# Kernel tuning notes

Measured on AMD Instinct MI355X. Metric: run time of the kernel, lower is better.

The kernel has to match this reference:

```python
import jax, jax.numpy as jnp
import numpy as np

B, T, C = 8, 1024, 1024
H, HS = 16, 64            # n_head, head_size
K, STRIDE = 32, 16        # block_length, stride_length
WIN = 128                 # local_window_size
EPS = 1e-5


def _ln(z, w):
    m = jnp.mean(z, axis=-1, keepdims=True)
    v = jnp.var(z, axis=-1, keepdims=True)
    return (z - m) / jnp.sqrt(v + EPS) * w


def setup_inputs() -> dict:
    key = jax.random.key(0)
    ks = jax.random.split(key, 8)
    s = 0.02
    return {
        "x": jax.random.normal(ks[0], (B, T, C), jnp.float32),
        "c_attn_w": jax.random.normal(ks[1], (3 * C, C), jnp.float32) * s,
        "conv_w": jax.random.normal(ks[2], (HS, HS, K), jnp.float32) * s,
        "ln_comp_w": jnp.ones((HS,), jnp.float32),
        "ln_local_w": jnp.ones((C,), jnp.float32),
        "gate_w1": jax.random.normal(ks[3], (C, 2 * C), jnp.float32) * s,
        "gate_ln_w": jnp.ones((C,), jnp.float32),
        "gate_w2": jax.random.normal(ks[4], (2, C), jnp.float32) * s,
        "c_proj_w": jax.random.normal(ks[5], (C, C), jnp.float32) * s,
    }


def reference(x, c_attn_w, conv_w, ln_comp_w, ln_local_w, gate_w1, gate_ln_w, gate_w2, c_proj_w):
    qkv = jnp.einsum('btc,oc->bto', x, c_attn_w)          # [B,T,3C]
    q, k, v = jnp.split(qkv, 3, axis=-1)
    def heads(t):
        return t.reshape(B, T, H, HS).transpose(0, 2, 1, 3)  # [B,H,T,hs]
    q, k, v = heads(q), heads(k), heads(v)

    # CompressionMLP: Conv1d over time + LayerNorm(hs) + exact GELU
    def compress(t):
        xr = t.transpose(0, 1, 3, 2).reshape(B * H, HS, T)   # [B*H, hs, T]
        co = jax.lax.conv_general_dilated(
            xr, conv_w, window_strides=(STRIDE,), padding='VALID',
            dimension_numbers=('NCH', 'OIH', 'NCH'))          # [B*H, hs, NB]
        co = co.transpose(0, 2, 1)                            # [B*H, NB, hs]
        co = jax.nn.gelu(_ln(co, ln_comp_w), approximate=False)
        nb = co.shape[1]
        return co.reshape(B, H, nb, HS)

    kc = compress(k)
    vc = compress(v)
    NB = kc.shape[2]  # 63
    scale = 1.0 / np.sqrt(HS)

    ti = jnp.arange(T)
    band = (ti[None, :] <= ti[:, None]) & (ti[None, :] >= ti[:, None] - WIN)  # [T,T]
    s_loc = jnp.einsum('bhqd,bhkd->bhqk', q, k) * scale
    s_loc = jnp.where(band[None, None], s_loc, -jnp.inf)
    local_out = jnp.einsum('bhqk,bhkd->bhqd', jax.nn.softmax(s_loc, axis=-1), v)
    local_out = local_out.transpose(0, 2, 1, 3).reshape(B, T, C)
    local_norm = _ln(local_out, ln_local_w)

    # compressed-KV attention with block-causal mask: block j <= token i
    bj = jnp.arange(NB)
    cmask = bj[None, :] <= ti[:, None]                        # [T,NB]
    s_cmp = jnp.einsum('bhqd,bhkd->bhqk', q, kc) * scale
    s_cmp = jnp.where(cmask[None, None], s_cmp, -jnp.inf)
    comp_out = jnp.einsum('bhqk,bhkd->bhqd', jax.nn.softmax(s_cmp, axis=-1), vc)
    comp_out = comp_out.transpose(0, 2, 1, 3).reshape(B, T, C)

    # AttentionGating: last-token features -> Linear -> LN -> ReLU -> Linear -> softmax
    feats = jnp.concatenate([local_norm[:, -1, :], comp_out[:, -1, :]], axis=-1)  # [B,2C]
    h = jax.nn.relu(_ln(feats @ gate_w1.T, gate_ln_w))
    gates = jax.nn.softmax(h @ gate_w2.T, axis=-1)            # [B,2]

    combined = gates[:, None, 0:1] * local_norm + gates[:, None, 1:2] * comp_out
    y = jnp.einsum('btc,oc->bto', combined, c_proj_w)
    return y
```

## Files before the change

kernel.cpp:

```cpp
#include <hip/hip_runtime.h>
#include <cstdint>
#include <cmath>
#include <cstddef>

typedef unsigned int u32;
typedef unsigned short u16;
typedef __bf16 bf16x8 __attribute__((ext_vector_type(8)));
typedef float f32x4 __attribute__((ext_vector_type(4)));
typedef u32 u32x4 __attribute__((ext_vector_type(4)));
typedef u32 u32x2 __attribute__((ext_vector_type(2)));

#define DEV static __device__ __forceinline__

DEV float bflo(u32 u) { return __uint_as_float(u << 16); }
DEV float bfhi(u32 u) { return __uint_as_float(u & 0xffff0000u); }
DEV u16 f2bf(float f) {
  u32 u = __float_as_uint(f);
  u += 0x7fffu + ((u >> 16) & 1u);
  return (u16)(u >> 16);
}
DEV f32x4 unpack_bf4(u32x2 r) {
  return (f32x4){bflo(r[0]), bfhi(r[0]), bflo(r[1]), bfhi(r[1])};
}
DEV float wredsum(float v) {
#pragma unroll
  for (int o = 32; o; o >>= 1) v += __shfl_xor(v, o, 64);
  return v;
}

DEV void gload_lds16(const u16* g, u16* lds_base) {
  __builtin_amdgcn_global_load_lds((const __attribute__((address_space(1))) void*)g,
                                   (__attribute__((address_space(3))) void*)lds_base,
                                   16, 0, 0);
}

__global__ __launch_bounds__(256) void fused_cast(const float* __restrict__ x,
                                                  const float* __restrict__ aw,
                                                  const float* __restrict__ pw,
                                                  const float* __restrict__ cw,
                                                  u16* __restrict__ xb,
                                                  u16* __restrict__ wab,
                                                  u16* __restrict__ wpb,
                                                  u16* __restrict__ wcb,
                                                  u16* __restrict__ kcb,
                                                  u16* __restrict__ vcb) {
  const int blk = blockIdx.x;
  if (blk < 12288) {
    const float* src;
    u16* dst;
    int base;
    if (blk < 8192) { src = x; dst = xb; base = blk; }
    else if (blk < 11264) { src = aw; dst = wab; base = blk - 8192; }
    else { src = pw; dst = wpb; base = blk - 11264; }
    const size_t idx = ((size_t)base * 256 + threadIdx.x) * 4;
    const f32x4 v = *(const f32x4*)&src[idx];
    u32x2 r;
    r[0] = (u32)f2bf(v[0]) | ((u32)f2bf(v[1]) << 16);
    r[1] = (u32)f2bf(v[2]) | ((u32)f2bf(v[3]) << 16);
    *(u32x2*)&dst[idx] = r;
  } else if (blk < 12800) {
    const int idx = (blk - 12288) * 256 + threadIdx.x;
    const int o = idx >> 11;
    const int rest = idx & 2047;
    const int i = rest >> 5;
    const int kk = rest & 31;
    wcb[(o << 11) + (kk << 6) + i] = f2bf(cw[idx]);
  } else {
    for (int i = threadIdx.x; i < 8192; i += 256) {
      const int bh = i >> 6, d = i & 63;
      kcb[bh * 4096 + 63 * 64 + d] = 0;
      vcb[bh * 4096 + d * 64 + 63] = 0;
    }
  }
}

template <int OUT_BF16>
__global__ __launch_bounds__(256, 4) void gemm_bt(const u16* __restrict__ A,
                                                  const u16* __restrict__ Bm,
                                                  void* __restrict__ out,
                                                  int M, int N, int K) {
  __shared__ u16 As[128 * 64];
  __shared__ u16 Bs[128 * 64];
  const int tid = threadIdx.x;
  const int lane = tid & 63;
  const int w = tid >> 6;
  const int row0 = blockIdx.x * 128;
  const int col0 = blockIdx.y * 128;
  const int wm = (w >> 1) * 64, wn = (w & 1) * 64;
  const int lr = lane & 15, lq = lane >> 4;
  const int srow = lane >> 3;
  const int scol = ((lane & 7) ^ (srow & 7)) * 8;
  const int pgA = ((lq ^ (lr & 7)) * 8);

  f32x4 acc[4][4] = {};

  for (int k0 = 0; k0 < K; k0 += 64) {
    __syncthreads();
#pragma unroll
    for (int c = 0; c < 4; ++c) {
      const int base_r = w * 32 + c * 8;
      gload_lds16(&A[(size_t)(row0 + base_r + srow) * K + k0 + scol], &As[base_r * 64]);
      gload_lds16(&Bm[(size_t)(col0 + base_r + srow) * K + k0 + scol], &Bs[base_r * 64]);
    }
    __syncthreads();
#pragma unroll
    for (int ks = 0; ks < 2; ++ks) {
      const int pg = pgA ^ (ks << 5);
      bf16x8 af[4], bfr[4];
#pragma unroll
      for (int i = 0; i < 4; ++i) {
        af[i] = *(const bf16x8*)&As[(wm + i * 16 + lr) * 64 + pg];
        bfr[i] = *(const bf16x8*)&Bs[(wn + i * 16 + lr) * 64 + pg];
      }
#pragma unroll
      for (int i = 0; i < 4; ++i)
#pragma unroll
        for (int j = 0; j < 4; ++j)
          acc[i][j] = __builtin_amdgcn_mfma_f32_16x16x32_bf16(af[i], bfr[j], acc[i][j], 0, 0, 0);
    }
  }
#pragma unroll
  for (int i = 0; i < 4; ++i)
#pragma unroll
    for (int j = 0; j < 4; ++j)
#pragma unroll
      for (int rr = 0; rr < 4; ++rr) {
        const int gr = row0 + wm + i * 16 + lq * 4 + rr;
        const int gc = col0 + wn + j * 16 + lr;
        const float v = acc[i][j][rr];
        if (OUT_BF16)
          ((u16*)out)[(size_t)gr * N + gc] = f2bf(v);
        else
          ((float*)out)[(size_t)gr * N + gc] = v;
      }
}

__global__ __launch_bounds__(256) void compress_kernel(const u16* __restrict__ qkv,
                                                       const u16* __restrict__ Wc,
                                                       const float* __restrict__ ln_w,
                                                       u16* __restrict__ kcb,
                                                       u16* __restrict__ vcb) {
  __shared__ u16 As[2][32 * 128];
  __shared__ u16 Bs[2][64 * 128];
  __shared__ float Cs[32][65];
  const int tid = threadIdx.x;
  const int lane = tid & 63, w = tid >> 6;
  const int lr = lane & 15, lq = lane >> 4;
  const int r0 = blockIdx.x * 32;
  const int srcoff = 1024 + (int)blockIdx.y * 1024;

  size_t abase[2];
#pragma unroll
  for (int g2 = 0; g2 < 2; ++g2) {
    const int r = 8 * w + 4 * g2 + (lane >> 4);
    const int gr = r0 + r;
    const int bh = gr / 63;
    const int nb = gr - bh * 63;
    const int b = bh >> 4, h = bh & 15;
    const int jbit = (lane >> 3) & 1;
    const int icol = ((lane & 7) ^ (r & 7)) * 8;
    abase[g2] = (size_t)(b * 1024 + nb * 16 + jbit) * 3072 + srcoff + h * 64 + icol;
  }
  size_t bbase[4];
#pragma unroll
  for (int c = 0; c < 4; ++c) {
    const int rB = 16 * w + 4 * c + (lane >> 4);
    const int Lcol = (((lane & 7) ^ (rB & 7)) | (lane & 8)) * 8;
    bbase[c] = (size_t)rB * 2048 + Lcol;
  }

  auto stage = [&](int it, int bs) {
#pragma unroll
    for (int g2 = 0; g2 < 2; ++g2)
      gload_lds16(&qkv[abase[g2] + (size_t)it * 6144], &As[bs][(8 * w + 4 * g2) * 128]);
#pragma unroll
    for (int c = 0; c < 4; ++c)
      gload_lds16(&Wc[bbase[c] + (size_t)it * 128], &Bs[bs][(16 * w + 4 * c) * 128]);
  };

  const int rw = (w & 1) * 16;
  const int cw = (w >> 1) * 32;
  f32x4 acc[2] = {};

  stage(0, 0);
  for (int it = 0; it < 16; ++it) {
    const int cur = it & 1;
    __syncthreads();
    if (it < 15) stage(it + 1, cur ^ 1);
    const int rowA = rw + lr;
#pragma unroll
    for (int ks = 0; ks < 4; ++ks) {
      const int L = ks * 4 + lq;
      const int pgA = (((L & 7) ^ (rowA & 7)) | (L & 8)) * 8;
      const bf16x8 af = *(const bf16x8*)&As[cur][rowA * 128 + pgA];
#pragma unroll
      for (int j = 0; j < 2; ++j) {
        const int rowB = cw + j * 16 + lr;
        const int pgB = (((L & 7) ^ (rowB & 7)) | (L & 8)) * 8;
        const bf16x8 bfr = *(const bf16x8*)&Bs[cur][rowB * 128 + pgB];
        acc[j] = __builtin_amdgcn_mfma_f32_16x16x32_bf16(af, bfr, acc[j], 0, 0, 0);
      }
    }
  }
  __syncthreads();
#pragma unroll
  for (int j = 0; j < 2; ++j)
#pragma unroll
    for (int rr = 0; rr < 4; ++rr)
      Cs[rw + lq * 4 + rr][cw + j * 16 + lr] = acc[j][rr];
  __syncthreads();
  if (tid < 32) {
    const int gr2 = r0 + tid;
    const int bh2 = gr2 / 63;
    const int nb2 = gr2 - bh2 * 63;
    float s = 0.f, s2 = 0.f;
#pragma unroll 8
    for (int d = 0; d < 64; ++d) {
      const float xv = Cs[tid][d];
      s += xv;
      s2 += xv * xv;
    }
    const float m = s * (1.f / 64.f);
    const float inv = rsqrtf(s2 * (1.f / 64.f) - m * m + 1e-5f);
    if (blockIdx.y == 0) {
      const size_t gb = (size_t)bh2 * 4096 + nb2 * 64;
#pragma unroll 8
      for (int d = 0; d < 64; ++d) {
        const float z = (Cs[tid][d] - m) * inv * ln_w[d];
        kcb[gb + d] = f2bf(0.5f * z * (1.f + erff(z * 0.70710678118f)));
      }
    } else {
      const size_t gb = (size_t)bh2 * 4096 + nb2;
#pragma unroll 8
      for (int d = 0; d < 64; ++d) {
        const float z = (Cs[tid][d] - m) * inv * ln_w[d];
        vcb[gb + d * 64] = f2bf(0.5f * z * (1.f + erff(z * 0.70710678118f)));
      }
    }
  }
}

__global__ __launch_bounds__(256, 4) void attn_fused(const u16* __restrict__ qkv,
                                                     const u16* __restrict__ kcb,
                                                     const u16* __restrict__ vcb,
                                                     u16* __restrict__ loc,
                                                     u16* __restrict__ outc) {
  __shared__ __align__(16) char smem[40448];
  u16* Ks = (u16*)smem;
  u16* Ps = (u16*)smem;
  u16* Vt = (u16*)(smem + 27648);
  u16* Kc = (u16*)smem;
  u16* Vc = (u16*)(smem + 9216);
  u16* Pc = (u16*)(smem + 18432);
  const int bh = blockIdx.x;
  const int b = bh >> 4, h = bh & 15;
  const int i0 = blockIdx.y * 64;
  const int jbase = i0 - 128;
  const int tid = threadIdx.x;
  const int lane = tid & 63, w = tid >> 6;
  const int lr = lane & 15, lq = lane >> 4;
  const int j3 = lane & 3;
  const int dh1 = (lane >> 2) & 1;

  u32x4 vreg[6];
#pragma unroll
  for (int c = 0; c < 6; ++c) {
    const int lin = c * 256 + tid;
    const int s = lin >> 3, d0 = (lin & 7) * 8;
    const int j = jbase + s;
    u32x4 kval = {0, 0, 0, 0}, vval = {0, 0, 0, 0};
    if (j >= 0) {
      const size_t ro = (size_t)(b * 1024 + j) * 3072 + h * 64 + d0;
      kval = *(const u32x4*)&qkv[ro + 1024];
      vval = *(const u32x4*)&qkv[ro + 2048];
    }
    vreg[c] = vval;
    *(u32x4*)&Ks[s * 72 + d0] = kval;
  }
  if (!dh1) {
    const int d0 = (lane & 7) * 8;
#pragma unroll
    for (int c = 0; c < 6; ++c) {
      const int s = (c * 256 + tid) >> 3;
      const int sc = (((s >> 3) ^ j3) << 3) + (s & 7);
      const u32x4 val = vreg[c];
#pragma unroll
      for (int q = 0; q < 4; ++q) {
        Vt[(d0 + 2 * q) * 200 + sc] = (u16)(val[q] & 0xffffu);
        Vt[(d0 + 2 * q + 1) * 200 + sc] = (u16)(val[q] >> 16);
      }
    }
  }
  bf16x8 qf[2];
  {
    const size_t qrow = (size_t)(b * 1024 + i0 + w * 16 + lr) * 3072 + h * 64;
#pragma unroll
    for (int ks = 0; ks < 2; ++ks) qf[ks] = *(const bf16x8*)&qkv[qrow + ks * 32 + lq * 8];
  }
  const size_t cb = (size_t)bh * 4096;
  u32x4 kcreg[2], vcreg[2];
#pragma unroll
  for (int c2 = 0; c2 < 2; ++c2) {
    const int i2 = c2 * 256 + tid;
    const size_t o2 = (size_t)(i2 >> 3) * 64 + (i2 & 7) * 8;
    kcreg[c2] = *(const u32x4*)&kcb[cb + o2];
    vcreg[c2] = *(const u32x4*)&vcb[cb + o2];
  }
  __syncthreads();

  f32x4 sa[9];
#pragma unroll
  for (int j9 = 0; j9 < 9; ++j9) sa[j9] = (f32x4){0.f, 0.f, 0.f, 0.f};
#pragma unroll
  for (int ks = 0; ks < 2; ++ks)
#pragma unroll
    for (int j9 = 0; j9 < 9; ++j9) {
      const int jt = w + j9;
      const bf16x8 kf = *(const bf16x8*)&Ks[(jt * 16 + lr) * 72 + ks * 32 + lq * 8];
      sa[j9] = __builtin_amdgcn_mfma_f32_16x16x32_bf16(qf[ks], kf, sa[j9], 0, 0, 0);
    }

  const float NINF = -__builtin_inff();
  float mx[4] = {NINF, NINF, NINF, NINF};
#pragma unroll
  for (int j9 = 0; j9 < 9; ++j9) {
    const int s = (w + j9) * 16 + lr;
#pragma unroll
    for (int rr = 0; rr < 4; ++rr) {
      const int qi = w * 16 + lq * 4 + rr;
      const bool valid = (jbase + s >= 0) && (s >= qi) && (s <= qi + 128);
      const float v = valid ? sa[j9][rr] * 0.125f : NINF;
      sa[j9][rr] = v;
      mx[rr] = fmaxf(mx[rr], v);
    }
  }
#pragma unroll
  for (int rr = 0; rr < 4; ++rr)
#pragma unroll
    for (int o = 1; o < 16; o <<= 1) mx[rr] = fmaxf(mx[rr], __shfl_xor(mx[rr], o, 64));
  float sum[4] = {0.f, 0.f, 0.f, 0.f};
#pragma unroll
  for (int j9 = 0; j9 < 9; ++j9)
#pragma unroll
    for (int rr = 0; rr < 4; ++rr) {
      const float p = __expf(sa[j9][rr] - mx[rr]);
      sa[j9][rr] = p;
      sum[rr] += p;
    }
#pragma unroll
  for (int rr = 0; rr < 4; ++rr) {
#pragma unroll
    for (int o = 1; o < 16; o <<= 1) sum[rr] += __shfl_xor(sum[rr], o, 64);
    sum[rr] = 1.0f / sum[rr];
  }
  __syncthreads();

#pragma unroll
  for (int j9 = 0; j9 < 9; ++j9) {
    const int jt = w + j9;
#pragma unroll
    for (int rr = 0; rr < 4; ++rr)
      Ps[(w * 16 + lq * 4 + rr) * 200 + jt * 16 + lr] = f2bf(sa[j9][rr] * sum[rr]);
  }
  {
    const int jz = (w == 0) ? 9 : (w == 1) ? 0 : (w == 2) ? 11 : 2;
#pragma unroll
    for (int rr = 0; rr < 4; ++rr) Ps[(w * 16 + lq * 4 + rr) * 200 + jz * 16 + lr] = 0;
  }
  __syncthreads();

  const int W = (w >> 1) * 32;
  const int G0 = W >> 3;
  f32x4 oa[4];
#pragma unroll
  for (int jt = 0; jt < 4; ++jt) oa[jt] = (f32x4){0.f, 0.f, 0.f, 0.f};
#pragma unroll
  for (int ks = 0; ks < 5; ++ks) {
    const bf16x8 pf = *(const bf16x8*)&Ps[(w * 16 + lr) * 200 + W + ks * 32 + lq * 8];
#pragma unroll
    for (int jl = 0; jl < 2; ++jl) {
      const int rl = jl * 16 + lr;
      const int g = G0 + ks * 4 + lq;
      const bf16x8 vf = *(const bf16x8*)&Vt[rl * 200 + ((g ^ (rl >> 3)) << 3)];
      oa[jl] = __builtin_amdgcn_mfma_f32_16x16x32_bf16(pf, vf, oa[jl], 0, 0, 0);
    }
  }
#pragma unroll
  for (int jt = 0; jt < 2; ++jt)
#pragma unroll
    for (int rr = 0; rr < 4; ++rr)
      loc[(size_t)(b * 1024 + i0 + w * 16 + lq * 4 + rr) * 1024 + h * 64 + jt * 16 + lr] =
          f2bf(oa[jt][rr]);
  __syncthreads();

  if (dh1) {
    const int d0 = (lane & 7) * 8 - 32;
#pragma unroll
    for (int c = 0; c < 6; ++c) {
      const int s = (c * 256 + tid) >> 3;
      const int sc = (((s >> 3) ^ j3) << 3) + (s & 7);
      const u32x4 val = vreg[c];
#pragma unroll
      for (int q = 0; q < 4; ++q) {
        Vt[(d0 + 2 * q) * 200 + sc] = (u16)(val[q] & 0xffffu);
        Vt[(d0 + 2 * q + 1) * 200 + sc] = (u16)(val[q] >> 16);
      }
    }
  }
  __syncthreads();

#pragma unroll
  for (int ks = 0; ks < 5; ++ks) {
    const bf16x8 pf = *(const bf16x8*)&Ps[(w * 16 + lr) * 200 + W + ks * 32 + lq * 8];
#pragma unroll
    for (int jl = 0; jl < 2; ++jl) {
      const int rl = jl * 16 + lr;
      const int g = G0 + ks * 4 + lq;
      const bf16x8 vf = *(const bf16x8*)&Vt[rl * 200 + ((g ^ (rl >> 3)) << 3)];
      oa[2 + jl] = __builtin_amdgcn_mfma_f32_16x16x32_bf16(pf, vf, oa[2 + jl], 0, 0, 0);
    }
  }
#pragma unroll
  for (int jt = 2; jt < 4; ++jt)
#pragma unroll
    for (int rr = 0; rr < 4; ++rr)
      loc[(size_t)(b * 1024 + i0 + w * 16 + lq * 4 + rr) * 1024 + h * 64 + jt * 16 + lr] =
          f2bf(oa[jt][rr]);

  __syncthreads();
#pragma unroll
  for (int c2 = 0; c2 < 2; ++c2) {
    const int i2 = c2 * 256 + tid;
    const int r2 = i2 >> 3, o2 = (i2 & 7) * 8;
    *(u32x4*)&Kc[r2 * 72 + o2] = kcreg[c2];
    *(u32x4*)&Vc[r2 * 72 + o2] = vcreg[c2];
  }
  __syncthreads();

  f32x4 ca[4];
#pragma unroll
  for (int j = 0; j < 4; ++j) ca[j] = (f32x4){0.f, 0.f, 0.f, 0.f};
#pragma unroll
  for (int ks = 0; ks < 2; ++ks)
#pragma unroll
    for (int j = 0; j < 4; ++j) {
      const bf16x8 kf = *(const bf16x8*)&Kc[(j * 16 + lr) * 72 + ks * 32 + lq * 8];
      ca[j] = __builtin_amdgcn_mfma_f32_16x16x32_bf16(qf[ks], kf, ca[j], 0, 0, 0);
    }
  float mc[4] = {NINF, NINF, NINF, NINF};
#pragma unroll
  for (int j = 0; j < 4; ++j) {
    const int s = j * 16 + lr;
#pragma unroll
    for (int rr = 0; rr < 4; ++rr) {
      const int i = i0 + w * 16 + lq * 4 + rr;
      const bool valid = (s <= i) && (s < 63);
      const float v = valid ? ca[j][rr] * 0.125f : NINF;
      ca[j][rr] = v;
      mc[rr] = fmaxf(mc[rr], v);
    }
  }
#pragma unroll
  for (int rr = 0; rr < 4; ++rr)
#pragma unroll
    for (int o = 1; o < 16; o <<= 1) mc[rr] = fmaxf(mc[rr], __shfl_xor(mc[rr], o, 64));
  float sc[4] = {0.f, 0.f, 0.f, 0.f};
#pragma unroll
  for (int j = 0; j < 4; ++j)
#pragma unroll
    for (int rr = 0; rr < 4; ++rr) {
      const float p = __expf(ca[j][rr] - mc[rr]);
      ca[j][rr] = p;
      sc[rr] += p;
    }
#pragma unroll
  for (int rr = 0; rr < 4; ++rr) {
#pragma unroll
    for (int o = 1; o < 16; o <<= 1) sc[rr] += __shfl_xor(sc[rr], o, 64);
    sc[rr] = 1.0f / sc[rr];
  }
#pragma unroll
  for (int j = 0; j < 4; ++j)
#pragma unroll
    for (int rr = 0; rr < 4; ++rr)
      Pc[(w * 16 + lq * 4 + rr) * 72 + j * 16 + lr] = f2bf(ca[j][rr] * sc[rr]);
  __syncthreads();

  f32x4 co[4];
#pragma unroll
  for (int jt = 0; jt < 4; ++jt) co[jt] = (f32x4){0.f, 0.f, 0.f, 0.f};
#pragma unroll
  for (int ks = 0; ks < 2; ++ks) {
    const bf16x8 pf = *(const bf16x8*)&Pc[(w * 16 + lr) * 72 + ks * 32 + lq * 8];
#pragma unroll
    for (int jt = 0; jt < 4; ++jt) {
      const bf16x8 vf = *(const bf16x8*)&Vc[(jt * 16 + lr) * 72 + ks * 32 + lq * 8];
      co[jt] = __builtin_amdgcn_mfma_f32_16x16x32_bf16(pf, vf, co[jt], 0, 0, 0);
    }
  }
#pragma unroll
  for (int jt = 0; jt < 4; ++jt)
#pragma unroll
    for (int rr = 0; rr < 4; ++rr)
      outc[(size_t)(b * 1024 + i0 + w * 16 + lq * 4 + rr) * 1024 + h * 64 + jt * 16 + lr] =
          f2bf(co[jt][rr]);
}

__global__ __launch_bounds__(256) void gate_gemv(const u16* __restrict__ locb,
                                                 const u16* __restrict__ compb,
                                                 const float* __restrict__ lnw,
                                                 const float* __restrict__ w1,
                                                 float* __restrict__ hraw) {
  __shared__ float sm[8], sinv[8];
  const int tid = threadIdx.x;
  const int w = tid >> 6, lane = tid & 63;
  for (int bb = w; bb < 8; bb += 4) {
    const u16* rp = &locb[((size_t)bb * 1024 + 1023) * 1024 + lane * 16];
    const u32x4 a0 = *(const u32x4*)rp;
    const u32x4 a1 = *(const u32x4*)(rp + 8);
    float s = 0.f, s2 = 0.f;
#pragma unroll
    for (int q = 0; q < 4; ++q) {
      const float x0 = bflo(a0[q]), x1 = bfhi(a0[q]);
      const float x2 = bflo(a1[q]), x3 = bfhi(a1[q]);
      s += x0 + x1 + x2 + x3;
      s2 += x0 * x0 + x1 * x1 + x2 * x2 + x3 * x3;
    }
    s = wredsum(s);
    s2 = wredsum(s2);
    if (!lane) {
      const float m = s * (1.f / 1024.f);
      sm[bb] = m;
      sinv[bb] = rsqrtf(s2 * (1.f / 1024.f) - m * m + 1e-5f);
    }
  }
  __syncthreads();

  const int o = blockIdx.x * 4 + w;
  const float* wr = &w1[(size_t)o * 2048];
  float acc[8] = {};
#pragma unroll
  for (int it = 0; it < 4; ++it) {
    const int c = (it * 64 + lane) * 4;
    const f32x4 wv = *(const f32x4*)&wr[c];
    const f32x4 lw = *(const f32x4*)&lnw[c];
#pragma unroll
    for (int b = 0; b < 8; ++b) {
      const f32x4 xv = unpack_bf4(*(const u32x2*)&locb[((size_t)b * 1024 + 1023) * 1024 + c]);
      const float mb = sm[b], ib = sinv[b];
      acc[b] += ((xv[0] - mb) * ib * lw[0]) * wv[0] + ((xv[1] - mb) * ib * lw[1]) * wv[1] +
                ((xv[2] - mb) * ib * lw[2]) * wv[2] + ((xv[3] - mb) * ib * lw[3]) * wv[3];
    }
  }
#pragma unroll
  for (int it = 4; it < 8; ++it) {
    const int c = (it * 64 + lane) * 4;
    const f32x4 wv = *(const f32x4*)&wr[c];
    const int c2 = c - 1024;
#pragma unroll
    for (int b = 0; b < 8; ++b) {
      const f32x4 fv = unpack_bf4(*(const u32x2*)&compb[((size_t)b * 1024 + 1023) * 1024 + c2]);
      acc[b] += fv[0] * wv[0] + fv[1] * wv[1] + fv[2] * wv[2] + fv[3] * wv[3];
    }
  }
#pragma unroll
  for (int b = 0; b < 8; ++b) acc[b] = wredsum(acc[b]);
  if (lane == 0) {
#pragma unroll
    for (int b = 0; b < 8; ++b) hraw[b * 1024 + o] = acc[b];
  }
}

__global__ __launch_bounds__(256) void gate_fin(const float* __restrict__ hraw,
                                                const float* __restrict__ lnw,
                                                const float* __restrict__ w2,
                                                float* __restrict__ gates) {
  const int b = blockIdx.x, tid = threadIdx.x;
  const f32x4 v = *(const f32x4*)&hraw[(size_t)b * 1024 + tid * 4];
  float s = v[0] + v[1] + v[2] + v[3];
  float s2 = v[0] * v[0] + v[1] * v[1] + v[2] * v[2] + v[3] * v[3];
  s = wredsum(s);
  s2 = wredsum(s2);
  __shared__ float rs[4], rs2[4];
  const int w = tid >> 6, lane = tid & 63;
  if (!lane) { rs[w] = s; rs2[w] = s2; }
  __syncthreads();
  s = rs[0] + rs[1] + rs[2] + rs[3];
  s2 = rs2[0] + rs2[1] + rs2[2] + rs2[3];
  const float m = s * (1.f / 1024.f);
  const float inv = rsqrtf(s2 * (1.f / 1024.f) - m * m + 1e-5f);
  float p0 = 0.f, p1 = 0.f;
#pragma unroll
  for (int k = 0; k < 4; ++k) {
    float hh = (v[k] - m) * inv * lnw[tid * 4 + k];
    hh = fmaxf(hh, 0.f);
    p0 += hh * w2[tid * 4 + k];
    p1 += hh * w2[1024 + tid * 4 + k];
  }
  p0 = wredsum(p0);
  p1 = wredsum(p1);
  __syncthreads();
  if (!lane) { rs[w] = p0; rs2[w] = p1; }
  __syncthreads();
  if (tid == 0) {
    const float l0 = rs[0] + rs[1] + rs[2] + rs[3];
    const float l1 = rs2[0] + rs2[1] + rs2[2] + rs2[3];
    const float mm = fmaxf(l0, l1);
    const float e0 = __expf(l0 - mm), e1 = __expf(l1 - mm);
    const float iv = 1.f / (e0 + e1);
    gates[b * 2] = e0 * iv;
    gates[b * 2 + 1] = e1 * iv;
  }
}

__global__ __launch_bounds__(256) void combine_ln_cast(const u16* __restrict__ locb,
                                                       const u16* __restrict__ compb,
                                                       const float* __restrict__ lnw,
                                                       const float* __restrict__ gates,
                                                       u16* __restrict__ outb) {
  const int row = blockIdx.x, tid = threadIdx.x;
  const size_t base = (size_t)row * 1024 + tid * 4;
  const f32x4 v = unpack_bf4(*(const u32x2*)&locb[base]);
  float s = v[0] + v[1] + v[2] + v[3];
  float s2 = v[0] * v[0] + v[1] * v[1] + v[2] * v[2] + v[3] * v[3];
  s = wredsum(s);
  s2 = wredsum(s2);
  __shared__ float rs[4], rs2[4];
  const int w = tid >> 6, lane = tid & 63;
  if (!lane) { rs[w] = s; rs2[w] = s2; }
  __syncthreads();
  s = rs[0] + rs[1] + rs[2] + rs[3];
  s2 = rs2[0] + rs2[1] + rs2[2] + rs2[3];
  const float m = s * (1.f / 1024.f);
  const float inv = rsqrtf(s2 * (1.f / 1024.f) - m * m + 1e-5f);
  const int b = row >> 10;
  const float g0 = gates[2 * b], g1 = gates[2 * b + 1];
  const f32x4 wv = *(const f32x4*)&lnw[tid * 4];
  const f32x4 c = unpack_bf4(*(const u32x2*)&compb[base]);
  float ov[4];
#pragma unroll
  for (int k = 0; k < 4; ++k) ov[k] = g0 * ((v[k] - m) * inv * wv[k]) + g1 * c[k];
  u32x2 r;
  r[0] = (u32)f2bf(ov[0]) | ((u32)f2bf(ov[1]) << 16);
  r[1] = (u32)f2bf(ov[2]) | ((u32)f2bf(ov[3]) << 16);
  *(u32x2*)&outb[base] = r;
}

extern "C" void kernel_launch(void* const* d_in, const int* in_sizes, int n_in,
                              void* d_out, int out_size, void* d_ws, size_t ws_size,
                              hipStream_t stream) {
  const float* x = (const float*)d_in[0];
  const float* c_attn_w = (const float*)d_in[1];
  const float* conv_w = (const float*)d_in[2];
  const float* ln_comp_w = (const float*)d_in[3];
  const float* ln_local_w = (const float*)d_in[4];
  const float* gate_w1 = (const float*)d_in[5];
  const float* gate_ln_w = (const float*)d_in[6];
  const float* gate_w2 = (const float*)d_in[7];
  const float* c_proj_w = (const float*)d_in[8];
  float* y = (float*)d_out;

  char* ws = (char*)d_ws;
  size_t off = 0;
  auto alloc = [&](size_t bytes) -> void* {
    void* p = ws + off;
    off += (bytes + 255) & ~(size_t)255;
    return p;
  };
  u16* qkvb = (u16*)alloc((size_t)8192 * 3072 * 2);
  u16* xb = (u16*)alloc((size_t)8192 * 1024 * 2);
  u16* wab = (u16*)alloc((size_t)3072 * 1024 * 2);
  u16* wpb = (u16*)alloc((size_t)1024 * 1024 * 2);
  u16* wcb = (u16*)alloc((size_t)64 * 2048 * 2);
  u16* kcb = (u16*)alloc((size_t)128 * 4096 * 2);
  u16* vcb = (u16*)alloc((size_t)128 * 4096 * 2);
  u16* locb = (u16*)alloc((size_t)8192 * 1024 * 2);
  u16* compb = (u16*)alloc((size_t)8192 * 1024 * 2);
  float* hraw = (float*)alloc((size_t)8192 * 4);
  float* gates = (float*)alloc(64);
  u16* combb = (u16*)alloc((size_t)8192 * 1024 * 2);

  fused_cast<<<12801, 256, 0, stream>>>(x, c_attn_w, c_proj_w, conv_w, xb, wab, wpb, wcb, kcb,
                                        vcb);

  gemm_bt<1><<<dim3(64, 24), 256, 0, stream>>>(xb, wab, qkvb, 8192, 3072, 1024);

  compress_kernel<<<dim3(252, 2), 256, 0, stream>>>(qkvb, wcb, ln_comp_w, kcb, vcb);

  attn_fused<<<dim3(128, 16), 256, 0, stream>>>(qkvb, kcb, vcb, locb, compb);

  gate_gemv<<<256, 256, 0, stream>>>(locb, compb, ln_local_w, gate_w1, hraw);
  gate_fin<<<8, 256, 0, stream>>>(hraw, gate_ln_w, gate_w2, gates);

  combine_ln_cast<<<8192, 256, 0, stream>>>(locb, compb, ln_local_w, gates, combb);

  gemm_bt<0><<<dim3(64, 8), 256, 0, stream>>>(combb, wpb, y, 8192, 1024, 1024);
}
```

Measured before the change: 282.1 us.

## Stage full transposed V once, drop intra-wave barriers, one-row-per-wave combine LN

The local attention kernel now grows LDS and writes the whole transposed V tile once, up front. This removes the two-phase V staging, its extra barriers and the register-held V copy, and the PV product runs over all four output tiles in a single pass. Two __syncthreads after per-wave P writes become compiler memory fences, because each wave reads only its own P rows. The combine/LayerNorm kernel now handles one row per wavefront with wider 16-element loads, which removes the shared-memory cross-wave reduction and its barrier. The larger LDS footprint may lower occupancy of the attention kernel, and the fence-only P handoff relies on wave-local visibility.

```diff
diff --git a/kernel.cpp b/kernel.cpp
--- a/kernel.cpp
+++ b/kernel.cpp
@@ -245,7 +245,7 @@
                                                      const u16* __restrict__ vcb,
                                                      u16* __restrict__ loc,
                                                      u16* __restrict__ outc) {
-  __shared__ __align__(16) char smem[40448];
+  __shared__ __align__(16) char smem[53248];
   u16* Ks = (u16*)smem;
   u16* Ps = (u16*)smem;
   u16* Vt = (u16*)(smem + 27648);
@@ -259,10 +259,7 @@
   const int tid = threadIdx.x;
   const int lane = tid & 63, w = tid >> 6;
   const int lr = lane & 15, lq = lane >> 4;
-  const int j3 = lane & 3;
-  const int dh1 = (lane >> 2) & 1;
-
-  u32x4 vreg[6];
+
 #pragma unroll
   for (int c = 0; c < 6; ++c) {
     const int lin = c * 256 + tid;
@@ -274,21 +271,12 @@
       kval = *(const u32x4*)&qkv[ro + 1024];
       vval = *(const u32x4*)&qkv[ro + 2048];
     }
-    vreg[c] = vval;
     *(u32x4*)&Ks[s * 72 + d0] = kval;
-  }
-  if (!dh1) {
-    const int d0 = (lane & 7) * 8;
-#pragma unroll
-    for (int c = 0; c < 6; ++c) {
-      const int s = (c * 256 + tid) >> 3;
-      const int sc = (((s >> 3) ^ j3) << 3) + (s & 7);
-      const u32x4 val = vreg[c];
-#pragma unroll
-      for (int q = 0; q < 4; ++q) {
-        Vt[(d0 + 2 * q) * 200 + sc] = (u16)(val[q] & 0xffffu);
-        Vt[(d0 + 2 * q + 1) * 200 + sc] = (u16)(val[q] >> 16);
-      }
+    const int sg = (((s >> 3) ^ (lane & 7)) << 3) | (s & 7);
+#pragma unroll
+    for (int q = 0; q < 4; ++q) {
+      Vt[(d0 + 2 * q) * 200 + sg] = (u16)(vval[q] & 0xffffu);
+      Vt[(d0 + 2 * q + 1) * 200 + sg] = (u16)(vval[q] >> 16);
     }
   }
   bf16x8 qf[2];
@@ -367,7 +355,7 @@
 #pragma unroll
     for (int rr = 0; rr < 4; ++rr) Ps[(w * 16 + lq * 4 + rr) * 200 + jz * 16 + lr] = 0;
   }
-  __syncthreads();
+  asm volatile("" ::: "memory");
 
   const int W = (w >> 1) * 32;
   const int G0 = W >> 3;
@@ -378,50 +366,15 @@
   for (int ks = 0; ks < 5; ++ks) {
     const bf16x8 pf = *(const bf16x8*)&Ps[(w * 16 + lr) * 200 + W + ks * 32 + lq * 8];
 #pragma unroll
-    for (int jl = 0; jl < 2; ++jl) {
-      const int rl = jl * 16 + lr;
+    for (int jt = 0; jt < 4; ++jt) {
+      const int rl = jt * 16 + lr;
       const int g = G0 + ks * 4 + lq;
       const bf16x8 vf = *(const bf16x8*)&Vt[rl * 200 + ((g ^ (rl >> 3)) << 3)];
-      oa[jl] = __builtin_amdgcn_mfma_f32_16x16x32_bf16(pf, vf, oa[jl], 0, 0, 0);
-    }
-  }
-#pragma unroll
-  for (int jt = 0; jt < 2; ++jt)
-#pragma unroll
-    for (int rr = 0; rr < 4; ++rr)
-      loc[(size_t)(b * 1024 + i0 + w * 16 + lq * 4 + rr) * 1024 + h * 64 + jt * 16 + lr] =
-          f2bf(oa[jt][rr]);
-  __syncthreads();
-
-  if (dh1) {
-    const int d0 = (lane & 7) * 8 - 32;
-#pragma unroll
-    for (int c = 0; c < 6; ++c) {
-      const int s = (c * 256 + tid) >> 3;
-      const int sc = (((s >> 3) ^ j3) << 3) + (s & 7);
-      const u32x4 val = vreg[c];
-#pragma unroll
-      for (int q = 0; q < 4; ++q) {
-        Vt[(d0 + 2 * q) * 200 + sc] = (u16)(val[q] & 0xffffu);
-        Vt[(d0 + 2 * q + 1) * 200 + sc] = (u16)(val[q] >> 16);
-      }
-    }
-  }
-  __syncthreads();
-
-#pragma unroll
-  for (int ks = 0; ks < 5; ++ks) {
-    const bf16x8 pf = *(const bf16x8*)&Ps[(w * 16 + lr) * 200 + W + ks * 32 + lq * 8];
-#pragma unroll
-    for (int jl = 0; jl < 2; ++jl) {
-      const int rl = jl * 16 + lr;
-      const int g = G0 + ks * 4 + lq;
-      const bf16x8 vf = *(const bf16x8*)&Vt[rl * 200 + ((g ^ (rl >> 3)) << 3)];
-      oa[2 + jl] = __builtin_amdgcn_mfma_f32_16x16x32_bf16(pf, vf, oa[2 + jl], 0, 0, 0);
-    }
-  }
-#pragma unroll
-  for (int jt = 2; jt < 4; ++jt)
+      oa[jt] = __builtin_amdgcn_mfma_f32_16x16x32_bf16(pf, vf, oa[jt], 0, 0, 0);
+    }
+  }
+#pragma unroll
+  for (int jt = 0; jt < 4; ++jt)
 #pragma unroll
     for (int rr = 0; rr < 4; ++rr)
       loc[(size_t)(b * 1024 + i0 + w * 16 + lq * 4 + rr) * 1024 + h * 64 + jt * 16 + lr] =
@@ -484,7 +437,7 @@
 #pragma unroll
     for (int rr = 0; rr < 4; ++rr)
       Pc[(w * 16 + lq * 4 + rr) * 72 + j * 16 + lr] = f2bf(ca[j][rr] * sc[rr]);
-  __syncthreads();
+  asm volatile("" ::: "memory");
 
   f32x4 co[4];
 #pragma unroll
@@ -618,32 +571,53 @@
                                                        const float* __restrict__ lnw,
                                                        const float* __restrict__ gates,
                                                        u16* __restrict__ outb) {
-  const int row = blockIdx.x, tid = threadIdx.x;
-  const size_t base = (size_t)row * 1024 + tid * 4;
-  const f32x4 v = unpack_bf4(*(const u32x2*)&locb[base]);
-  float s = v[0] + v[1] + v[2] + v[3];
-  float s2 = v[0] * v[0] + v[1] * v[1] + v[2] * v[2] + v[3] * v[3];
+  const int w = threadIdx.x >> 6, lane = threadIdx.x & 63;
+  const int row = blockIdx.x * 4 + w;
+  const size_t base = (size_t)row * 1024 + lane * 16;
+  const u32x4 a0 = *(const u32x4*)&locb[base];
+  const u32x4 a1 = *(const u32x4*)&locb[base + 8];
+  float xv[16];
+#pragma unroll
+  for (int q = 0; q < 4; ++q) {
+    xv[2 * q] = bflo(a0[q]);
+    xv[2 * q + 1] = bfhi(a0[q]);
+    xv[8 + 2 * q] = bflo(a1[q]);
+    xv[8 + 2 * q + 1] = bfhi(a1[q]);
+  }
+  float s = 0.f, s2 = 0.f;
+#pragma unroll
+  for (int k = 0; k < 16; ++k) {
+    s += xv[k];
+    s2 += xv[k] * xv[k];
+  }
   s = wredsum(s);
   s2 = wredsum(s2);
-  __shared__ float rs[4], rs2[4];
-  const int w = tid >> 6, lane = tid & 63;
-  if (!lane) { rs[w] = s; rs2[w] = s2; }
-  __syncthreads();
-  s = rs[0] + rs[1] + rs[2] + rs[3];
-  s2 = rs2[0] + rs2[1] + rs2[2] + rs2[3];
   const float m = s * (1.f / 1024.f);
   const float inv = rsqrtf(s2 * (1.f / 1024.f) - m * m + 1e-5f);
   const int b = row >> 10;
   const float g0 = gates[2 * b], g1 = gates[2 * b + 1];
-  const f32x4 wv = *(const f32x4*)&lnw[tid * 4];
-  const f32x4 c = unpack_bf4(*(const u32x2*)&compb[base]);
-  float ov[4];
-#pragma unroll
-  for (int k = 0; k < 4; ++k) ov[k] = g0 * ((v[k] - m) * inv * wv[k]) + g1 * c[k];
-  u32x2 r;
-  r[0] = (u32)f2bf(ov[0]) | ((u32)f2bf(ov[1]) << 16);
-  r[1] = (u32)f2bf(ov[2]) | ((u32)f2bf(ov[3]) << 16);
-  *(u32x2*)&outb[base] = r;
+  const u32x4 c0 = *(const u32x4*)&compb[base];
+  const u32x4 c1 = *(const u32x4*)&compb[base + 8];
+  const f32x4 lw0 = *(const f32x4*)&lnw[lane * 16];
+  const f32x4 lw1 = *(const f32x4*)&lnw[lane * 16 + 4];
+  const f32x4 lw2 = *(const f32x4*)&lnw[lane * 16 + 8];
+  const f32x4 lw3 = *(const f32x4*)&lnw[lane * 16 + 12];
+  u32x4 r0, r1;
+#pragma unroll
+  for (int q = 0; q < 4; ++q) {
+    const float lwa = (q < 2) ? lw0[2 * q] : lw1[2 * q - 4];
+    const float lwb = (q < 2) ? lw0[2 * q + 1] : lw1[2 * q - 3];
+    const float lwc = (q < 2) ? lw2[2 * q] : lw3[2 * q - 4];
+    const float lwd = (q < 2) ? lw2[2 * q + 1] : lw3[2 * q - 3];
+    const float o0 = g0 * ((xv[2 * q] - m) * inv * lwa) + g1 * bflo(c0[q]);
+    const float o1 = g0 * ((xv[2 * q + 1] - m) * inv * lwb) + g1 * bfhi(c0[q]);
+    const float o2 = g0 * ((xv[8 + 2 * q] - m) * inv * lwc) + g1 * bflo(c1[q]);
+    const float o3 = g0 * ((xv[8 + 2 * q + 1] - m) * inv * lwd) + g1 * bfhi(c1[q]);
+    r0[q] = (u32)f2bf(o0) | ((u32)f2bf(o1) << 16);
+    r1[q] = (u32)f2bf(o2) | ((u32)f2bf(o3) << 16);
+  }
+  *(u32x4*)&outb[base] = r0;
+  *(u32x4*)&outb[base + 8] = r1;
 }
 
 extern "C" void kernel_launch(void* const* d_in, const int* in_sizes, int n_in,
@@ -692,7 +666,7 @@
   gate_gemv<<<256, 256, 0, stream>>>(locb, compb, ln_local_w, gate_w1, hraw);
   gate_fin<<<8, 256, 0, stream>>>(hraw, gate_ln_w, gate_w2, gates);
 
-  combine_ln_cast<<<8192, 256, 0, stream>>>(locb, compb, ln_local_w, gates, combb);
+  combine_ln_cast<<<2048, 256, 0, stream>>>(locb, compb, ln_local_w, gates, combb);
 
   gemm_bt<0><<<dim3(64, 8), 256, 0, stream>>>(combb, wpb, y, 8192, 1024, 1024);
 }
```

Result: faster. 272.7 us (-3.3%).
